# Kernel optimization log

Hardware: AMD Instinct MI355X
Metric: run time of the kernel (lower is better)

The kernel has to match this reference:

```python
import jax, jax.numpy as jnp
import numpy as np


def setup_inputs() -> dict:
    key = jax.random.key(0)
    k1, k2, k3 = jax.random.split(key, 3)
    N, L, S, H, D = 2, 2048, 2048, 8, 64
    return {
        "queries": jax.random.normal(k1, (N, L, H, D), dtype=jnp.float32),
        "keys": jax.random.normal(k2, (N, S, H, D), dtype=jnp.float32),
        "values": jax.random.normal(k3, (N, S, H, D), dtype=jnp.float32),
        "q_mask": jnp.ones((N, L), dtype=bool),
        "kv_mask": jnp.ones((N, S), dtype=bool),
    }


def reference(queries, keys, values, q_mask, kv_mask):
    # QK^T: [N, L, S, H]
    qk = jnp.einsum("nlhd,nshd->nlsh", queries, keys)
    # mask: True where attention is allowed
    mask = q_mask[:, :, None, None] & kv_mask[:, None, :, None]
    qk = jnp.where(mask, qk, -jnp.inf)
    softmax_temp = 1.0 / np.sqrt(queries.shape[3]).astype(np.float32)
    A = jax.nn.softmax(softmax_temp * qk, axis=2)  # over S
    out = jnp.einsum("nlsh,nshd->nlhd", A, values)
    return out
```

## Files before the change

### kernel.cpp

```cpp
#include <hip/hip_runtime.h>
#include <hip/hip_bf16.h>

#define N_B 2
#define L_Q 2048
#define S_K 2048
#define N_H 8
#define D_H 64
#define HD  512
#define KVB 64
#define NT  (S_K / KVB)
#define RS  72
#define LOG2E 1.4426950408889634f

typedef __attribute__((ext_vector_type(8))) short bf16x8;
typedef __attribute__((ext_vector_type(4))) short short4v;
typedef __attribute__((ext_vector_type(4))) float f32x4;

__device__ __forceinline__ short f2bf(float f) {
  union { float f; unsigned u; } v; v.f = f;
  return (short)((v.u + 0x7FFFu + ((v.u >> 16) & 1u)) >> 16);
}
__device__ __forceinline__ float bf2f(short s) {
  union { unsigned u; float f; } w; w.u = ((unsigned)(unsigned short)s) << 16;
  return w.f;
}
__device__ __forceinline__ bf16x8 pack8(float4 a, float4 b) {
  bf16x8 t;
  t[0]=f2bf(a.x); t[1]=f2bf(a.y); t[2]=f2bf(a.z); t[3]=f2bf(a.w);
  t[4]=f2bf(b.x); t[5]=f2bf(b.y); t[6]=f2bf(b.z); t[7]=f2bf(b.w);
  return t;
}

__global__ __launch_bounds__(256)
void preconv_kernel(const float* __restrict__ K, const float* __restrict__ V,
                    const int* __restrict__ kvm,
                    short* __restrict__ kws, short* __restrict__ vws,
                    unsigned long long* __restrict__ mws) {
  const size_t i = (size_t)blockIdx.x * 256 + threadIdx.x;
  const float4* kp = (const float4*)K + i * 2;
  float4 a = kp[0], b = kp[1];
  *(bf16x8*)(kws + i * 8) = pack8(a, b);
  const float4* vp = (const float4*)V + i * 2;
  float4 c = vp[0], d = vp[1];
  *(bf16x8*)(vws + i * 8) = pack8(c, d);
  if (blockIdx.x == 0 && threadIdx.x < (N_B * S_K / 64)) {
    const int* src = kvm + threadIdx.x * 64;
    unsigned long long m = 0;
    #pragma unroll 8
    for (int bb = 0; bb < 64; ++bb) m |= (src[bb] ? 1ull : 0ull) << bb;
    mws[threadIdx.x] = m;
  }
}

__global__ __launch_bounds__(128, 2)
void attn_fwd_v2(const float* __restrict__ Q, const short* __restrict__ Kb,
                 const short* __restrict__ Vb,
                 const unsigned long long* __restrict__ mbits,
                 float* __restrict__ Out) {
  __shared__ __align__(128) short kt[2 * 4096];
  __shared__ __align__(128) short vt[2 * 4096];
  __shared__ __align__(16)  short pl[2][16 * RS];

  const int tid  = threadIdx.x;
  const int wid  = tid >> 6;
  const int lane = tid & 63;
  const int l16  = lane & 15;
  const int lg   = lane >> 4;

  const int logical = ((blockIdx.x & 7) << 7) | (blockIdx.x >> 3);
  const int nh = logical >> 6;
  const int qb = logical & 63;
  const int n  = nh >> 3;
  const int h  = nh & 7;
  const int q0 = qb * 32 + wid * 16;

  const float* Qn = Q  + ((size_t)n * L_Q) * HD + h * D_H;
  const char*  Kn = (const char*)(Kb + ((size_t)n * S_K) * HD + h * D_H);
  const char*  Vn = (const char*)(Vb + ((size_t)n * S_K) * HD + h * D_H);

  int koffb[4], voffb[4];
  #pragma unroll
  for (int i = 0; i < 4; ++i) {
    const int p   = wid * 4096 + i * 1024 + lane * 16;
    const int row = p >> 7;
    const int cb  = (p & 127) ^ ((row & 7) << 4);
    koffb[i] = row * 1024 + cb;
    const int k  = ((p >> 9) << 2) | ((p >> 5) & 3);
    const int d  = (((p >> 7) & 3) << 4) | ((p >> 1) & 15);
    voffb[i] = k * 1024 + d * 2;
  }

  bf16x8 qf[2];
  {
    const float* qp = Qn + (size_t)(q0 + l16) * HD + lg * 8;
    #pragma unroll
    for (int c = 0; c < 2; ++c) {
      float4 a = *(const float4*)(qp + c * 32);
      float4 b = *(const float4*)(qp + c * 32 + 4);
      float4 as, bs;
      as.x=a.x*0.125f; as.y=a.y*0.125f; as.z=a.z*0.125f; as.w=a.w*0.125f;
      bs.x=b.x*0.125f; bs.y=b.y*0.125f; bs.z=b.z*0.125f; bs.w=b.w*0.125f;
      qf[c] = pack8(as, bs);
    }
  }

  const int swz    = (l16 & 7) << 4;
  const int kaddrA = l16 * 128 + ((lg * 16) ^ swz);
  const int kaddrB = l16 * 128 + ((64 + lg * 16) ^ swz);
  const int vlane  = lg * 1024 + l16 * 8;
  const unsigned kt0 = (unsigned)(size_t)(__attribute__((address_space(3))) char*)((char*)&kt[0]);
  const unsigned vt0 = (unsigned)(size_t)(__attribute__((address_space(3))) char*)((char*)&vt[0]);

  f32x4 o[4];
  #pragma unroll
  for (int g = 0; g < 4; ++g) o[g] = (f32x4){0.f, 0.f, 0.f, 0.f};
  float m_run[4], l_run[4];
  #pragma unroll
  for (int r = 0; r < 4; ++r) { m_run[r] = -3e38f; l_run[r] = 0.f; }

  short* pw = pl[wid];

  #define ISSUE(t_) do {                                                          \
    const int bs_ = ((t_) & 1) * 8192;                                            \
    const char* ks_ = Kn + (size_t)(t_) * 65536;                                  \
    const char* vs_ = Vn + (size_t)(t_) * 65536;                                  \
    _Pragma("unroll")                                                             \
    for (int i_ = 0; i_ < 4; ++i_) {                                              \
      __builtin_amdgcn_global_load_lds(                                           \
        (const __attribute__((address_space(1))) void*)(ks_ + koffb[i_]),         \
        (__attribute__((address_space(3))) void*)((char*)kt + bs_ + wid*4096 + i_*1024), \
        16, 0, 0);                                                                \
      __builtin_amdgcn_global_load_lds(                                           \
        (const __attribute__((address_space(1))) void*)(vs_ + voffb[i_]),         \
        (__attribute__((address_space(3))) void*)((char*)vt + bs_ + wid*4096 + i_*1024), \
        16, 0, 0);                                                                \
    }                                                                             \
  } while (0)

  ISSUE(0);

  for (int t = 0; t < NT; ++t) {
    __syncthreads();
    if (t + 1 < NT) ISSUE(t + 1);
    const int bo = (t & 1) * 8192;

    f32x4 sc[4];
    #pragma unroll
    for (int g = 0; g < 4; ++g) {
      bf16x8 kb0 = *(const bf16x8*)((const char*)kt + bo + g * 2048 + kaddrA);
      bf16x8 kb1 = *(const bf16x8*)((const char*)kt + bo + g * 2048 + kaddrB);
      f32x4 z = (f32x4){0.f, 0.f, 0.f, 0.f};
      z = __builtin_amdgcn_mfma_f32_16x16x32_bf16(qf[0], kb0, z, 0, 0, 0);
      z = __builtin_amdgcn_mfma_f32_16x16x32_bf16(qf[1], kb1, z, 0, 0, 0);
      sc[g] = z;
    }

    const unsigned long long mb = mbits[n * NT + t];
    #pragma unroll
    for (int g = 0; g < 4; ++g) {
      if (!((mb >> (g * 16 + l16)) & 1ull)) {
        #pragma unroll
        for (int r = 0; r < 4; ++r) sc[g][r] = -3e38f;
      }
    }

    float mt[4];
    #pragma unroll
    for (int r = 0; r < 4; ++r) {
      float v = fmaxf(fmaxf(sc[0][r], sc[1][r]), fmaxf(sc[2][r], sc[3][r]));
      v = fmaxf(v, __shfl_xor(v, 1));
      v = fmaxf(v, __shfl_xor(v, 2));
      v = fmaxf(v, __shfl_xor(v, 4));
      v = fmaxf(v, __shfl_xor(v, 8));
      mt[r] = v;
    }
    float alpha[4];
    #pragma unroll
    for (int r = 0; r < 4; ++r) {
      float mn = fmaxf(m_run[r], mt[r]);
      alpha[r] = __builtin_amdgcn_exp2f((m_run[r] - mn) * LOG2E);
      m_run[r] = mn;
    }
    float rsum[4] = {0.f, 0.f, 0.f, 0.f};
    short pb[4][4];
    #pragma unroll
    for (int g = 0; g < 4; ++g) {
      #pragma unroll
      for (int r = 0; r < 4; ++r) {
        float p = __builtin_amdgcn_exp2f((sc[g][r] - m_run[r]) * LOG2E);
        short s = f2bf(p);
        pb[g][r] = s;
        rsum[r] += bf2f(s);
      }
    }
    #pragma unroll
    for (int r = 0; r < 4; ++r) {
      float v = rsum[r];
      v += __shfl_xor(v, 1);
      v += __shfl_xor(v, 2);
      v += __shfl_xor(v, 4);
      v += __shfl_xor(v, 8);
      l_run[r] = l_run[r] * alpha[r] + v;
    }
    #pragma unroll
    for (int g = 0; g < 4; ++g) {
      f32x4 tv = o[g];
      #pragma unroll
      for (int r = 0; r < 4; ++r) tv[r] *= alpha[r];
      o[g] = tv;
    }

    #pragma unroll
    for (int g = 0; g < 4; ++g)
      #pragma unroll
      for (int r = 0; r < 4; ++r)
        pw[(lg * 4 + r) * RS + g * 16 + l16] = pb[g][r];

    bf16x8 pa0 = *(const bf16x8*)&pw[l16 * RS + lg * 8];
    bf16x8 pa1 = *(const bf16x8*)&pw[l16 * RS + 32 + lg * 8];

    const unsigned va = vt0 + (unsigned)(bo + vlane);
    #define TRRD(dst, off) asm volatile("ds_read_b64_tr_b16 %0, %1 offset:" off \
                                        : "=v"(dst) : "v"(va))
    short4v w0la, w0lb, w0ha, w0hb, w1la, w1lb, w1ha, w1hb;
    short4v w2la, w2lb, w2ha, w2hb, w3la, w3lb, w3ha, w3hb;
    TRRD(w0la, "0");   TRRD(w0lb, "512"); TRRD(w0ha, "4096"); TRRD(w0hb, "4608");
    TRRD(w1la, "128"); TRRD(w1lb, "640"); TRRD(w1ha, "4224"); TRRD(w1hb, "4736");
    TRRD(w2la, "256"); TRRD(w2lb, "768"); TRRD(w2ha, "4352"); TRRD(w2hb, "4864");
    TRRD(w3la, "384"); TRRD(w3lb, "896"); TRRD(w3ha, "4480"); TRRD(w3hb, "4992");
    asm volatile("s_waitcnt lgkmcnt(0)" ::: "memory");
    __builtin_amdgcn_sched_barrier(0);

    bf16x8 v0l = __builtin_shufflevector(w0la, w0lb, 0,1,2,3,4,5,6,7);
    bf16x8 v0h = __builtin_shufflevector(w0ha, w0hb, 0,1,2,3,4,5,6,7);
    bf16x8 v1l = __builtin_shufflevector(w1la, w1lb, 0,1,2,3,4,5,6,7);
    bf16x8 v1h = __builtin_shufflevector(w1ha, w1hb, 0,1,2,3,4,5,6,7);
    bf16x8 v2l = __builtin_shufflevector(w2la, w2lb, 0,1,2,3,4,5,6,7);
    bf16x8 v2h = __builtin_shufflevector(w2ha, w2hb, 0,1,2,3,4,5,6,7);
    bf16x8 v3l = __builtin_shufflevector(w3la, w3lb, 0,1,2,3,4,5,6,7);
    bf16x8 v3h = __builtin_shufflevector(w3ha, w3hb, 0,1,2,3,4,5,6,7);

    o[0] = __builtin_amdgcn_mfma_f32_16x16x32_bf16(pa0, v0l, o[0], 0, 0, 0);
    o[0] = __builtin_amdgcn_mfma_f32_16x16x32_bf16(pa1, v0h, o[0], 0, 0, 0);
    o[1] = __builtin_amdgcn_mfma_f32_16x16x32_bf16(pa0, v1l, o[1], 0, 0, 0);
    o[1] = __builtin_amdgcn_mfma_f32_16x16x32_bf16(pa1, v1h, o[1], 0, 0, 0);
    o[2] = __builtin_amdgcn_mfma_f32_16x16x32_bf16(pa0, v2l, o[2], 0, 0, 0);
    o[2] = __builtin_amdgcn_mfma_f32_16x16x32_bf16(pa1, v2h, o[2], 0, 0, 0);
    o[3] = __builtin_amdgcn_mfma_f32_16x16x32_bf16(pa0, v3l, o[3], 0, 0, 0);
    o[3] = __builtin_amdgcn_mfma_f32_16x16x32_bf16(pa1, v3h, o[3], 0, 0, 0);
  }

  float* op = Out + ((size_t)n * L_Q + q0) * HD + h * D_H;
  float inv[4];
  #pragma unroll
  for (int r = 0; r < 4; ++r) inv[r] = 1.0f / l_run[r];
  #pragma unroll
  for (int gd = 0; gd < 4; ++gd)
    #pragma unroll
    for (int r = 0; r < 4; ++r)
      op[(size_t)(lg * 4 + r) * HD + gd * 16 + l16] = o[gd][r] * inv[r];
}

__global__ __launch_bounds__(256, 2)
void attn_fwd_kernel(const float* __restrict__ Q, const float* __restrict__ K,
                     const float* __restrict__ V,
                     const int* __restrict__ q_mask,
                     const int* __restrict__ kv_mask,
                     float* __restrict__ Out) {
  __shared__ __align__(16) short kts[KVB * RS];
  __shared__ __align__(16) short vts[D_H * RS];
  __shared__ __align__(16) short pls[4][16 * RS];
  const int tid = threadIdx.x, wid = tid >> 6, lane = tid & 63;
  const int l16 = lane & 15, lg = lane >> 4;
  const int bid = blockIdx.x, nh = bid >> 5, qb = bid & 31;
  const int n = nh >> 3, h = nh & 7, q0 = qb * 64 + wid * 16;
  const float* Qb = Q + ((size_t)n * L_Q) * HD + h * D_H;
  const float* Kb = K + ((size_t)n * S_K) * HD + h * D_H;
  const float* Vb = V + ((size_t)n * S_K) * HD + h * D_H;
  const int* km = kv_mask + (size_t)n * S_K;
  (void)q_mask;
  bf16x8 qf[2];
  {
    const float* qp = Qb + (size_t)(q0 + l16) * HD + lg * 8;
    #pragma unroll
    for (int c = 0; c < 2; ++c) {
      float4 a = *(const float4*)(qp + c * 32);
      float4 b = *(const float4*)(qp + c * 32 + 4);
      float4 as, bs;
      as.x=a.x*0.125f; as.y=a.y*0.125f; as.z=a.z*0.125f; as.w=a.w*0.125f;
      bs.x=b.x*0.125f; bs.y=b.y*0.125f; bs.z=b.z*0.125f; bs.w=b.w*0.125f;
      qf[c] = pack8(as, bs);
    }
  }
  f32x4 o[4];
  #pragma unroll
  for (int g = 0; g < 4; ++g) o[g] = (f32x4){0.f, 0.f, 0.f, 0.f};
  float m_run[4], l_run[4];
  #pragma unroll
  for (int r = 0; r < 4; ++r) { m_run[r] = -3e38f; l_run[r] = 0.f; }
  for (int s0 = 0; s0 < S_K; s0 += KVB) {
    __syncthreads();
    {
      const int cid = tid << 1, row = cid >> 3, c0 = cid & 7;
      const float* kp = Kb + (size_t)(s0 + row) * HD + c0 * 8;
      float4 f0 = *(const float4*)(kp), f1 = *(const float4*)(kp + 4);
      float4 f2 = *(const float4*)(kp + 8), f3 = *(const float4*)(kp + 12);
      *(bf16x8*)&kts[row * RS + c0 * 8]     = pack8(f0, f1);
      *(bf16x8*)&kts[row * RS + c0 * 8 + 8] = pack8(f2, f3);
    }
    {
      const int kv = tid >> 2, dc = tid & 3;
      const float* vp = Vb + (size_t)(s0 + kv) * HD + dc * 16;
      float4 f0 = *(const float4*)(vp), f1 = *(const float4*)(vp + 4);
      float4 f2 = *(const float4*)(vp + 8), f3 = *(const float4*)(vp + 12);
      float tv[16] = { f0.x,f0.y,f0.z,f0.w, f1.x,f1.y,f1.z,f1.w,
                       f2.x,f2.y,f2.z,f2.w, f3.x,f3.y,f3.z,f3.w };
      short* dst = &vts[(dc * 16) * RS + kv];
      #pragma unroll
      for (int j = 0; j < 16; ++j) dst[j * RS] = f2bf(tv[j]);
    }
    __syncthreads();
    f32x4 sc[4];
    #pragma unroll
    for (int g = 0; g < 4; ++g) {
      bf16x8 kb0 = *(const bf16x8*)&kts[(g*16 + l16) * RS + lg * 8];
      bf16x8 kb1 = *(const bf16x8*)&kts[(g*16 + l16) * RS + 32 + lg * 8];
      f32x4 z = (f32x4){0.f, 0.f, 0.f, 0.f};
      z = __builtin_amdgcn_mfma_f32_16x16x32_bf16(qf[0], kb0, z, 0, 0, 0);
      z = __builtin_amdgcn_mfma_f32_16x16x32_bf16(qf[1], kb1, z, 0, 0, 0);
      sc[g] = z;
    }
    #pragma unroll
    for (int g = 0; g < 4; ++g) {
      float b = km[s0 + g*16 + l16] ? 0.f : -3e38f;
      #pragma unroll
      for (int r = 0; r < 4; ++r) sc[g][r] += b;
    }
    float mt[4];
    #pragma unroll
    for (int r = 0; r < 4; ++r) {
      float v = fmaxf(fmaxf(sc[0][r], sc[1][r]), fmaxf(sc[2][r], sc[3][r]));
      v = fmaxf(v, __shfl_xor(v, 1)); v = fmaxf(v, __shfl_xor(v, 2));
      v = fmaxf(v, __shfl_xor(v, 4)); v = fmaxf(v, __shfl_xor(v, 8));
      mt[r] = v;
    }
    float alpha[4];
    #pragma unroll
    for (int r = 0; r < 4; ++r) {
      float mn = fmaxf(m_run[r], mt[r]);
      alpha[r] = __builtin_amdgcn_exp2f((m_run[r] - mn) * LOG2E);
      m_run[r] = mn;
    }
    float rsum[4] = {0.f, 0.f, 0.f, 0.f};
    short pb[4][4];
    #pragma unroll
    for (int g = 0; g < 4; ++g)
      #pragma unroll
      for (int r = 0; r < 4; ++r) {
        float p = __builtin_amdgcn_exp2f((sc[g][r] - m_run[r]) * LOG2E);
        short s = f2bf(p); pb[g][r] = s; rsum[r] += bf2f(s);
      }
    #pragma unroll
    for (int r = 0; r < 4; ++r) {
      float v = rsum[r];
      v += __shfl_xor(v, 1); v += __shfl_xor(v, 2);
      v += __shfl_xor(v, 4); v += __shfl_xor(v, 8);
      l_run[r] = l_run[r] * alpha[r] + v;
    }
    #pragma unroll
    for (int g = 0; g < 4; ++g)
      #pragma unroll
      for (int r = 0; r < 4; ++r) o[g][r] *= alpha[r];
    short* pwf = pls[wid];
    #pragma unroll
    for (int g = 0; g < 4; ++g)
      #pragma unroll
      for (int r = 0; r < 4; ++r)
        pwf[(lg*4 + r) * RS + g*16 + l16] = pb[g][r];
    __syncthreads();
    bf16x8 pa0 = *(const bf16x8*)&pwf[l16 * RS + lg * 8];
    bf16x8 pa1 = *(const bf16x8*)&pwf[l16 * RS + 32 + lg * 8];
    #pragma unroll
    for (int gd = 0; gd < 4; ++gd) {
      bf16x8 vb0 = *(const bf16x8*)&vts[(gd*16 + l16) * RS + lg * 8];
      bf16x8 vb1 = *(const bf16x8*)&vts[(gd*16 + l16) * RS + 32 + lg * 8];
      o[gd] = __builtin_amdgcn_mfma_f32_16x16x32_bf16(pa0, vb0, o[gd], 0, 0, 0);
      o[gd] = __builtin_amdgcn_mfma_f32_16x16x32_bf16(pa1, vb1, o[gd], 0, 0, 0);
    }
  }
  float* op = Out + ((size_t)n * L_Q + q0) * HD + h * D_H;
  float inv[4];
  #pragma unroll
  for (int r = 0; r < 4; ++r) inv[r] = 1.0f / l_run[r];
  #pragma unroll
  for (int gd = 0; gd < 4; ++gd)
    #pragma unroll
    for (int r = 0; r < 4; ++r)
      op[(size_t)(lg*4 + r) * HD + gd*16 + l16] = o[gd][r] * inv[r];
}

extern "C" void kernel_launch(void* const* d_in, const int* in_sizes, int n_in,
                              void* d_out, int out_size, void* d_ws, size_t ws_size,
                              hipStream_t stream) {
  const float* Q = (const float*)d_in[0];
  const float* K = (const float*)d_in[1];
  const float* V = (const float*)d_in[2];
  const int* qm = (const int*)d_in[3];
  const int* km = (const int*)d_in[4];
  float* Out = (float*)d_out;
  (void)in_sizes; (void)n_in; (void)out_size;

  const size_t kbytes = (size_t)N_B * S_K * HD * 2;
  const size_t need = 2 * kbytes + 512;
  if (ws_size >= need) {
    short* kws = (short*)d_ws;
    short* vws = (short*)((char*)d_ws + kbytes);
    unsigned long long* mws = (unsigned long long*)((char*)d_ws + 2 * kbytes);
    hipLaunchKernelGGL(preconv_kernel, dim3(1024), dim3(256), 0, stream,
                       K, V, km, kws, vws, mws);
    hipLaunchKernelGGL(attn_fwd_v2, dim3(1024), dim3(128), 0, stream,
                       Q, kws, vws, mws, Out);
  } else {
    hipLaunchKernelGGL(attn_fwd_kernel, dim3(512), dim3(256), 0, stream,
                       Q, K, V, qm, km, Out);
  }
}
```

Measured before the change: 147.0 us.

## Split KV range in two with 4-wave blocks and add a combine kernel

```diff
diff --git a/kernel.cpp b/kernel.cpp
--- a/kernel.cpp
+++ b/kernel.cpp
@@ -8,8 +8,9 @@
 #define D_H 64
 #define HD  512
 #define KVB 64
-#define NT  (S_K / KVB)
+#define NT  32
 #define RS  72
+#define PQT ((size_t)N_B * L_Q * N_H)
 #define LOG2E 1.4426950408889634f
 
 typedef __attribute__((ext_vector_type(8))) short bf16x8;
@@ -52,14 +53,16 @@
   }
 }
 
-__global__ __launch_bounds__(128, 2)
-void attn_fwd_v2(const float* __restrict__ Q, const short* __restrict__ Kb,
+__global__ __launch_bounds__(256, 3)
+void attn_fwd_v3(const float* __restrict__ Q, const short* __restrict__ Kb,
                  const short* __restrict__ Vb,
                  const unsigned long long* __restrict__ mbits,
-                 float* __restrict__ Out) {
+                 float* __restrict__ Out,
+                 float* __restrict__ Ow, float* __restrict__ Mw,
+                 float* __restrict__ Lw, int split) {
   __shared__ __align__(128) short kt[2 * 4096];
   __shared__ __align__(128) short vt[2 * 4096];
-  __shared__ __align__(16)  short pl[2][16 * RS];
+  __shared__ __align__(16)  short pl[4][16 * RS];
 
   const int tid  = threadIdx.x;
   const int wid  = tid >> 6;
@@ -67,21 +70,25 @@
   const int l16  = lane & 15;
   const int lg   = lane >> 4;
 
-  const int logical = ((blockIdx.x & 7) << 7) | (blockIdx.x >> 3);
-  const int nh = logical >> 6;
-  const int qb = logical & 63;
+  const int per_xcd = gridDim.x >> 3;
+  const int logical = (blockIdx.x & 7) * per_xcd + (blockIdx.x >> 3);
+  int nh, sp, qb;
+  if (split == 2) { nh = logical >> 6; sp = (logical >> 5) & 1; qb = logical & 31; }
+  else            { nh = logical >> 5; sp = 0;                  qb = logical & 31; }
   const int n  = nh >> 3;
   const int h  = nh & 7;
-  const int q0 = qb * 32 + wid * 16;
-
-  const float* Qn = Q  + ((size_t)n * L_Q) * HD + h * D_H;
+  const int q0 = qb * 64 + wid * 16;
+  const int tps = (split == 2) ? (NT / 2) : NT;
+  const int t0 = sp * tps, t1 = t0 + tps;
+
+  const float* Qn = Q + ((size_t)n * L_Q) * HD + h * D_H;
   const char*  Kn = (const char*)(Kb + ((size_t)n * S_K) * HD + h * D_H);
   const char*  Vn = (const char*)(Vb + ((size_t)n * S_K) * HD + h * D_H);
 
-  int koffb[4], voffb[4];
-  #pragma unroll
-  for (int i = 0; i < 4; ++i) {
-    const int p   = wid * 4096 + i * 1024 + lane * 16;
+  int koffb[2], voffb[2];
+  #pragma unroll
+  for (int i = 0; i < 2; ++i) {
+    const int p   = (wid * 2 + i) * 1024 + lane * 16;
     const int row = p >> 7;
     const int cb  = (p & 127) ^ ((row & 7) << 4);
     koffb[i] = row * 1024 + cb;
@@ -108,7 +115,6 @@
   const int kaddrA = l16 * 128 + ((lg * 16) ^ swz);
   const int kaddrB = l16 * 128 + ((64 + lg * 16) ^ swz);
   const int vlane  = lg * 1024 + l16 * 8;
-  const unsigned kt0 = (unsigned)(size_t)(__attribute__((address_space(3))) char*)((char*)&kt[0]);
   const unsigned vt0 = (unsigned)(size_t)(__attribute__((address_space(3))) char*)((char*)&vt[0]);
 
   f32x4 o[4];
@@ -125,23 +131,23 @@
     const char* ks_ = Kn + (size_t)(t_) * 65536;                                  \
     const char* vs_ = Vn + (size_t)(t_) * 65536;                                  \
     _Pragma("unroll")                                                             \
-    for (int i_ = 0; i_ < 4; ++i_) {                                              \
+    for (int i_ = 0; i_ < 2; ++i_) {                                              \
       __builtin_amdgcn_global_load_lds(                                           \
         (const __attribute__((address_space(1))) void*)(ks_ + koffb[i_]),         \
-        (__attribute__((address_space(3))) void*)((char*)kt + bs_ + wid*4096 + i_*1024), \
+        (__attribute__((address_space(3))) void*)((char*)kt + bs_ + (wid*2+i_)*1024), \
         16, 0, 0);                                                                \
       __builtin_amdgcn_global_load_lds(                                           \
         (const __attribute__((address_space(1))) void*)(vs_ + voffb[i_]),         \
-        (__attribute__((address_space(3))) void*)((char*)vt + bs_ + wid*4096 + i_*1024), \
+        (__attribute__((address_space(3))) void*)((char*)vt + bs_ + (wid*2+i_)*1024), \
         16, 0, 0);                                                                \
     }                                                                             \
   } while (0)
 
-  ISSUE(0);
-
-  for (int t = 0; t < NT; ++t) {
+  ISSUE(t0);
+
+  for (int t = t0; t < t1; ++t) {
     __syncthreads();
-    if (t + 1 < NT) ISSUE(t + 1);
+    if (t + 1 < t1) ISSUE(t + 1);
     const int bo = (t & 1) * 8192;
 
     f32x4 sc[4];
@@ -250,15 +256,49 @@
     o[3] = __builtin_amdgcn_mfma_f32_16x16x32_bf16(pa1, v3h, o[3], 0, 0, 0);
   }
 
-  float* op = Out + ((size_t)n * L_Q + q0) * HD + h * D_H;
-  float inv[4];
-  #pragma unroll
-  for (int r = 0; r < 4; ++r) inv[r] = 1.0f / l_run[r];
-  #pragma unroll
-  for (int gd = 0; gd < 4; ++gd)
-    #pragma unroll
-    for (int r = 0; r < 4; ++r)
-      op[(size_t)(lg * 4 + r) * HD + gd * 16 + l16] = o[gd][r] * inv[r];
+  if (split == 2) {
+    #pragma unroll
+    for (int r = 0; r < 4; ++r) {
+      const size_t row = ((size_t)n * L_Q + q0 + lg * 4 + r) * N_H + h;
+      const size_t ob  = ((size_t)sp * PQT + row) * D_H;
+      #pragma unroll
+      for (int gd = 0; gd < 4; ++gd)
+        Ow[ob + gd * 16 + l16] = o[gd][r];
+      if (l16 == 0) { Mw[sp * PQT + row] = m_run[r]; Lw[sp * PQT + row] = l_run[r]; }
+    }
+  } else {
+    float* op = Out + ((size_t)n * L_Q + q0) * HD + h * D_H;
+    float inv[4];
+    #pragma unroll
+    for (int r = 0; r < 4; ++r) inv[r] = 1.0f / l_run[r];
+    #pragma unroll
+    for (int gd = 0; gd < 4; ++gd)
+      #pragma unroll
+      for (int r = 0; r < 4; ++r)
+        op[(size_t)(lg * 4 + r) * HD + gd * 16 + l16] = o[gd][r] * inv[r];
+  }
+}
+
+__global__ __launch_bounds__(256)
+void combine_kernel(const float* __restrict__ Ow, const float* __restrict__ Mw,
+                    const float* __restrict__ Lw, float* __restrict__ Out) {
+  const int gid = blockIdx.x * 256 + threadIdx.x;
+  const size_t rid = (size_t)(gid >> 4);
+  const int d0 = (gid & 15) << 2;
+  float m0 = Mw[rid],       l0 = Lw[rid];
+  float m1 = Mw[PQT + rid], l1 = Lw[PQT + rid];
+  float M  = fmaxf(m0, m1);
+  float w0 = __builtin_amdgcn_exp2f((m0 - M) * LOG2E);
+  float w1 = __builtin_amdgcn_exp2f((m1 - M) * LOG2E);
+  float inv = 1.0f / (l0 * w0 + l1 * w1);
+  const float4 o0 = *(const float4*)(Ow + rid * D_H + d0);
+  const float4 o1 = *(const float4*)(Ow + (PQT + rid) * D_H + d0);
+  float4 r;
+  r.x = (o0.x * w0 + o1.x * w1) * inv;
+  r.y = (o0.y * w0 + o1.y * w1) * inv;
+  r.z = (o0.z * w0 + o1.z * w1) * inv;
+  r.w = (o0.w * w0 + o1.w * w1) * inv;
+  *(float4*)(Out + rid * D_H + d0) = r;
 }
 
 __global__ __launch_bounds__(256, 2)
@@ -410,16 +450,31 @@
   float* Out = (float*)d_out;
   (void)in_sizes; (void)n_in; (void)out_size;
 
-  const size_t kbytes = (size_t)N_B * S_K * HD * 2;
-  const size_t need = 2 * kbytes + 512;
-  if (ws_size >= need) {
+  const size_t kbytes  = (size_t)N_B * S_K * HD * 2;
+  const size_t need1   = 2 * kbytes + 1024;
+  const size_t owbytes = 2 * PQT * D_H * sizeof(float);
+  const size_t mlbytes = 2 * PQT * sizeof(float);
+  const size_t need2   = need1 + owbytes + 2 * mlbytes;
+
+  if (ws_size >= need1) {
     short* kws = (short*)d_ws;
     short* vws = (short*)((char*)d_ws + kbytes);
     unsigned long long* mws = (unsigned long long*)((char*)d_ws + 2 * kbytes);
     hipLaunchKernelGGL(preconv_kernel, dim3(1024), dim3(256), 0, stream,
                        K, V, km, kws, vws, mws);
-    hipLaunchKernelGGL(attn_fwd_v2, dim3(1024), dim3(128), 0, stream,
-                       Q, kws, vws, mws, Out);
+    if (ws_size >= need2) {
+      float* Ow = (float*)((char*)d_ws + need1);
+      float* Mw = (float*)((char*)d_ws + need1 + owbytes);
+      float* Lw = (float*)((char*)d_ws + need1 + owbytes + mlbytes);
+      hipLaunchKernelGGL(attn_fwd_v3, dim3(1024), dim3(256), 0, stream,
+                         Q, kws, vws, mws, Out, Ow, Mw, Lw, 2);
+      hipLaunchKernelGGL(combine_kernel, dim3(2048), dim3(256), 0, stream,
+                         Ow, Mw, Lw, Out);
+    } else {
+      hipLaunchKernelGGL(attn_fwd_v3, dim3(512), dim3(256), 0, stream,
+                         Q, kws, vws, mws, Out, (float*)d_ws, (float*)d_ws,
+                         (float*)d_ws, 1);
+    }
   } else {
     hipLaunchKernelGGL(attn_fwd_kernel, dim3(512), dim3(256), 0, stream,
                        Q, K, V, qm, km, Out);
```

Result: no change. 148.1 us (+0.7%).
